# Kernel optimization log

Measured on AMD Instinct MI355X. Metric: run time of the kernel, lower is better.

The kernel has to match this reference:

```python
import jax, jax.numpy as jnp
import numpy as np

N_HEAD = 16
WINDOW = 16  # fixed_window_size


def setup_inputs() -> dict:
    key = jax.random.key(0)
    k1, k2, k3 = jax.random.split(key, 3)
    B, T, C = 2, 2048, 1024
    x = jax.random.normal(k1, (B, T, C), dtype=jnp.float32)
    # torch Linear(C, 3C, bias=False): y = x @ W.T with W [3C, C].
    # We store the pre-transposed [C, 3C] matrix so y = x @ w_qkv.
    w_qkv = jax.random.normal(k2, (C, 3 * C), dtype=jnp.float32) * (1.0 / np.sqrt(C))
    w_proj = jax.random.normal(k3, (C, C), dtype=jnp.float32) * (1.0 / np.sqrt(C))
    return {"x": x, "w_qkv": w_qkv, "w_proj": w_proj}


def reference(x, w_qkv, w_proj):
    B, T, C = x.shape
    H, D = N_HEAD, C // N_HEAD
    qkv = x @ w_qkv  # [B, T, 3C]
    q, k, v = jnp.split(qkv, 3, axis=-1)
    # [B, T, C] -> [B, H, T, D]
    q, k, v = (t.reshape(B, T, H, D).transpose(0, 2, 1, 3) for t in (q, k, v))
    att = jnp.einsum("bhtd,bhsd->bhts", q, k) * (1.0 / np.sqrt(D))  # [B,H,T,T]
    # Mask exactly as the torch module builds it: tril ones, then zero where
    # col - row >= fixed_window_size (note: col-row, per the source).
    row = jnp.arange(T)[:, None]
    col = jnp.arange(T)[None, :]
    mask = (col <= row) & ~(col - row >= WINDOW)  # [T, T] bool
    att = jnp.where(mask[None, None, :, :], att, -jnp.inf)
    att = jax.nn.softmax(att, axis=-1)
    y = jnp.einsum("bhts,bhsd->bhtd", att, v)  # [B,H,T,D]
    y = y.transpose(0, 2, 1, 3).reshape(B, T, C)
    return y @ w_proj
```

## Files before the change

### kernel.cpp

```cpp
#include <hip/hip_runtime.h>
#include <stdint.h>

#define LOG2E 1.4426950408889634f
#define QSCALE 0.18033688011112042f

typedef __attribute__((ext_vector_type(8))) short bf16x8;
typedef __attribute__((ext_vector_type(4))) float f32x4;
typedef __attribute__((ext_vector_type(8))) unsigned short u16x8;

#define B_ 2
#define T_ 2048
#define C_ 1024
#define H_ 16
#define D_ 64
#define BT_ 4096
#define N3_ 3072

#if __has_builtin(__builtin_amdgcn_exp2f)
#define EXP2(x) __builtin_amdgcn_exp2f(x)
#else
#define EXP2(x) exp2f(x)
#endif

__device__ __forceinline__ unsigned short f2bf(float f) {
  union { float f; unsigned u; } x; x.f = f;
  return (unsigned short)((x.u + 0x7fffu + ((x.u >> 16) & 1u)) >> 16);
}
__device__ __forceinline__ float bf2f(unsigned short u) {
  union { unsigned u; float f; } x; x.u = ((unsigned)u) << 16;
  return x.f;
}
__device__ __forceinline__ unsigned f2u(float f) {
  union { float f; unsigned u; } x; x.f = f; return x.u;
}
__device__ __forceinline__ unsigned pack_bf2(float a, float b) {
  return __builtin_amdgcn_perm(f2u(b) + 0x8000u, f2u(a) + 0x8000u, 0x07060302u);
}

__device__ __forceinline__ void gld16(const unsigned short* g, unsigned short* l) {
  __builtin_amdgcn_global_load_lds(
      (const __attribute__((address_space(1))) unsigned int*)g,
      (__attribute__((address_space(3))) unsigned int*)l, 16, 0, 0);
}

__device__ __forceinline__ void tr32(const float* __restrict__ in,
                                     unsigned short* __restrict__ out,
                                     int K, int N, int b, int nbx, int tid) {
  __shared__ unsigned short tile[32][33];
  const int bx = b % nbx, by = b / nbx;
  const int n0 = bx * 32, k0 = by * 32;
  const int tx = tid & 31, ty = (tid >> 5) * 4;
#pragma unroll
  for (int r = 0; r < 4; r++)
    tile[ty + r][tx] = f2bf(in[(size_t)(k0 + ty + r) * N + n0 + tx]);
  __syncthreads();
#pragma unroll
  for (int r = 0; r < 4; r++)
    out[(size_t)(n0 + ty + r) * K + k0 + tx] = tile[tx][ty + r];
}

__global__ __launch_bounds__(256) void prep_kernel(
    const float* __restrict__ x, unsigned short* __restrict__ xb,
    const float* __restrict__ wq, unsigned short* __restrict__ wqT,
    const float* __restrict__ wp, unsigned short* __restrict__ wpT) {
  const int bid = blockIdx.x, tid = threadIdx.x;
  if (bid < 4096) {
    int i = (bid * 256 + tid) * 4;
    float4 v = *(const float4*)(x + i);
    ushort4 o;
    o.x = f2bf(v.x); o.y = f2bf(v.y); o.z = f2bf(v.z); o.w = f2bf(v.w);
    *(ushort4*)(xb + i) = o;
  } else if (bid < 4096 + 3072) {
    tr32(wq, wqT, 1024, 3072, bid - 4096, 96, tid);
  } else {
    tr32(wp, wpT, 1024, 1024, bid - 7168, 32, tid);
  }
}

__device__ __forceinline__ void stage128(const unsigned short* __restrict__ G,
                                         unsigned short* L, int k, int tid) {
#pragma unroll
  for (int j = 0; j < 2; j++) {
    const int s = tid + 512 * j;
    const int row = s >> 3, ch = s & 7;
    gld16(G + (size_t)row * 1024 + k + ((ch ^ (row & 7)) * 8), L + s * 8);
  }
}

__global__ __launch_bounds__(512, 2) void gemm1_kernel(
    const unsigned short* __restrict__ A, const unsigned short* __restrict__ Bt,
    unsigned short* __restrict__ qo, unsigned short* __restrict__ ko,
    unsigned short* __restrict__ vo) {
  __shared__ unsigned short As[2][256 * 64];
  __shared__ unsigned short Bs[2][256 * 64];
  const int tid = threadIdx.x;
  const int wid = tid >> 6, lane = tid & 63;
  const int quad = lane >> 4, l16 = lane & 15;
  const int wm = (wid >> 2) * 128, wn = (wid & 3) * 64;

  const int id = blockIdx.x;
  const int swz = (id & 7) * 24 + (id >> 3);
  const int mb = swz / 12, nb = swz % 12;
  const int m0 = mb * 256, n0 = nb * 256;

  f32x4 acc[8][4] = {};

  stage128(A + (size_t)m0 * 1024,         &As[0][0],    0, tid);
  stage128(A + (size_t)(m0 + 128) * 1024, &As[0][8192], 0, tid);
  stage128(Bt + (size_t)n0 * 1024,        &Bs[0][0],    0, tid);
  stage128(Bt + (size_t)(n0 + 128) * 1024,&Bs[0][8192], 0, tid);

  for (int kt = 0; kt < 16; kt++) {
    const int cur = kt & 1;
    const int knext = (kt + 1) * 64;
#pragma unroll
    for (int p = 0; p < 4; p++) {
      if (kt < 15) {
        if (p == 0)
          stage128(A + (size_t)m0 * 1024, &As[cur ^ 1][0], knext, tid);
        else if (p == 1)
          stage128(A + (size_t)(m0 + 128) * 1024, &As[cur ^ 1][8192], knext, tid);
        else if (p == 2)
          stage128(Bt + (size_t)n0 * 1024, &Bs[cur ^ 1][0], knext, tid);
        else
          stage128(Bt + (size_t)(n0 + 128) * 1024, &Bs[cur ^ 1][8192], knext, tid);
      }
      if (p == 0) {
        if (kt < 15) asm volatile("s_waitcnt vmcnt(2)" ::: "memory");
        else         asm volatile("s_waitcnt vmcnt(0)" ::: "memory");
      }
      __builtin_amdgcn_s_barrier();
      __builtin_amdgcn_sched_barrier(0);

      const int mh = p >> 1, nh = p & 1;
      bf16x8 af[4][2], bfr[2][2];
#pragma unroll
      for (int mi = 0; mi < 4; mi++) {
        const int row = wm + (mh * 4 + mi) * 16 + l16;
        const int sw = row & 7;
#pragma unroll
        for (int ks = 0; ks < 2; ks++)
          af[mi][ks] = *(const bf16x8*)(&As[cur][0] + row * 64 + (((ks * 4 + quad) ^ sw) * 8));
      }
#pragma unroll
      for (int ni = 0; ni < 2; ni++) {
        const int row = wn + (nh * 2 + ni) * 16 + l16;
        const int sw = row & 7;
#pragma unroll
        for (int ks = 0; ks < 2; ks++)
          bfr[ni][ks] = *(const bf16x8*)(&Bs[cur][0] + row * 64 + (((ks * 4 + quad) ^ sw) * 8));
      }

      __builtin_amdgcn_s_setprio(1);
#pragma unroll
      for (int ks = 0; ks < 2; ks++)
#pragma unroll
        for (int mi = 0; mi < 4; mi++)
#pragma unroll
          for (int ni = 0; ni < 2; ni++)
            acc[mh * 4 + mi][nh * 2 + ni] = __builtin_amdgcn_mfma_f32_16x16x32_bf16(
                af[mi][ks], bfr[ni][ks], acc[mh * 4 + mi][nh * 2 + ni], 0, 0, 0);
      __builtin_amdgcn_s_setprio(0);
      __builtin_amdgcn_s_barrier();
    }
  }

  const int part = n0 >> 10;
  const int hh = ((n0 + wn) >> 6) & 15;
#pragma unroll
  for (int mi8 = 0; mi8 < 8; mi8++) {
#pragma unroll
    for (int r = 0; r < 4; r++) {
      const int m = m0 + wm + mi8 * 16 + quad * 4 + r;
      const int b = m >> 11, t = m & 2047;
#pragma unroll
      for (int ni = 0; ni < 4; ni++) {
        const int d = ni * 16 + l16;
        float val = acc[mi8][ni][r];
        if (part == 0) val *= QSCALE;
        const unsigned short bv = f2bf(val);
        if (part == 0)
          qo[((size_t)(b * H_ + hh) * T_ + t) * D_ + d] = bv;
        else if (part == 1)
          ko[((size_t)(b * H_ + hh) * T_ + t) * D_ + d] = bv;
        else
          vo[((size_t)(b * H_ + hh) * D_ + d) * T_ + t] = bv;
      }
    }
  }
}

__global__ __launch_bounds__(512) void gemm2_kernel(
    const unsigned short* __restrict__ A, const unsigned short* __restrict__ Bt,
    float* __restrict__ fo) {
  __shared__ unsigned short As[2][128 * 64];
  __shared__ unsigned short Bs[2][64 * 64];
  const int tid = threadIdx.x;
  const int wave = tid >> 6, lane = tid & 63;
  const int quad = lane >> 4, l16 = lane & 15;
  const int grp = wave >> 2, w4 = wave & 3;
  const int wm = (w4 >> 1) * 64, wn = (w4 & 1) * 32;
  const int m0 = blockIdx.y * 128, n0 = blockIdx.x * 64;
  const int gtid = tid & 255;

  f32x4 acc[4][2] = {};
  const int kbase = grp * 512;
  unsigned short* Asg = &As[grp][0];
  unsigned short* Bsg = &Bs[grp][0];

  for (int kk = 0; kk < 512; kk += 64) {
    const int k = kbase + kk;
    __syncthreads();
#pragma unroll
    for (int i = 0; i < 4; i++) {
      const int s = gtid + 256 * i;
      const int row = s >> 3, ch = s & 7;
      gld16(A + (size_t)(m0 + row) * 1024 + k + ((ch ^ (row & 7)) * 8), Asg + s * 8);
    }
#pragma unroll
    for (int i = 0; i < 2; i++) {
      const int s = gtid + 256 * i;
      const int row = s >> 3, ch = s & 7;
      gld16(Bt + (size_t)(n0 + row) * 1024 + k + ((ch ^ (row & 7)) * 8), Bsg + s * 8);
    }
    __syncthreads();
#pragma unroll
    for (int sub = 0; sub < 2; sub++) {
      bf16x8 af[4], bfr[2];
#pragma unroll
      for (int mi = 0; mi < 4; mi++) {
        const int row = wm + mi * 16 + l16;
        af[mi] = *(const bf16x8*)(Asg + row * 64 + (((sub * 4 + quad) ^ (row & 7)) * 8));
      }
#pragma unroll
      for (int ni = 0; ni < 2; ni++) {
        const int row = wn + ni * 16 + l16;
        bfr[ni] = *(const bf16x8*)(Bsg + row * 64 + (((sub * 4 + quad) ^ (row & 7)) * 8));
      }
#pragma unroll
      for (int mi = 0; mi < 4; mi++)
#pragma unroll
        for (int ni = 0; ni < 2; ni++)
          acc[mi][ni] = __builtin_amdgcn_mfma_f32_16x16x32_bf16(af[mi], bfr[ni], acc[mi][ni], 0, 0, 0);
    }
  }

  __syncthreads();
  float* comb = (float*)&As[0][0];
  if (grp == 1) {
#pragma unroll
    for (int mi = 0; mi < 4; mi++)
#pragma unroll
      for (int ni = 0; ni < 2; ni++)
        *(f32x4*)(comb + ((w4 * 8 + mi * 2 + ni) * 256 + lane * 4)) = acc[mi][ni];
  }
  __syncthreads();
  if (grp == 0) {
#pragma unroll
    for (int mi = 0; mi < 4; mi++) {
#pragma unroll
      for (int ni = 0; ni < 2; ni++) {
        f32x4 oth = *(const f32x4*)(comb + ((w4 * 8 + mi * 2 + ni) * 256 + lane * 4));
        f32x4 v = acc[mi][ni] + oth;
#pragma unroll
        for (int r = 0; r < 4; r++) {
          const int m = m0 + wm + mi * 16 + quad * 4 + r;
          fo[(size_t)m * 1024 + n0 + wn + ni * 16 + l16] = v[r];
        }
      }
    }
  }
}

__global__ __launch_bounds__(256) void attn_kernel(
    const unsigned short* __restrict__ qb, const unsigned short* __restrict__ kb,
    const unsigned short* __restrict__ vb, unsigned short* __restrict__ yb,
    unsigned short* __restrict__ po, float* __restrict__ pl) {
  const int tid = threadIdx.x;
  const int wave = tid >> 6, lane = tid & 63;
  const int quad = lane >> 4, l16 = lane & 15;

  const int bid = blockIdx.x;
  const int bh = bid & 31;
  const int u = 62 - (bid >> 5);
  int qs, c, nch;
  if (u < 11) { qs = u; c = 0; nch = 1; }
  else if (u < 33) { int v = u - 11; qs = 11 + (v >> 1); c = v & 1; nch = 2; }
  else { int v = u - 33; qs = 22 + v / 3; c = v % 3; nch = 3; }
  const int nt = qs + 1;
  const int j0 = c * nt / nch, j1 = (c + 1) * nt / nch;
  const int b = bh >> 4, h = bh & 15;

  __shared__ unsigned short Ks[64 * 64];
  __shared__ unsigned short Vt[64 * 64];
  __shared__ unsigned short Ps[4 * 16 * 68];
  unsigned short* Pw = Ps + wave * 16 * 68;

  const unsigned short* Qg = qb + (size_t)bh * T_ * D_;
  const unsigned short* Kg = kb + (size_t)bh * T_ * D_;
  const unsigned short* Vg = vb + (size_t)bh * D_ * T_;

  const unsigned short* qp = Qg + (size_t)(qs * 64 + wave * 16 + l16) * D_ + quad * 8;
  bf16x8 qf0 = *(const bf16x8*)qp, qf1 = *(const bf16x8*)(qp + 32);

  f32x4 o[4] = {};
  float lacc = 0.f;
  const int qglob = qs * 64 + wave * 16 + l16;
  const int sloc_base = quad * 4;

  const int trow = tid >> 3, tch = tid & 7;

  for (int jt = j0; jt < j1; jt++) {
    const int s0 = jt * 64;
    __syncthreads();
    {
      const int r0 = trow, r1 = trow + 32;
      gld16(Kg + (size_t)(s0 + r0) * D_ + ((tch ^ (r0 & 7)) * 8), Ks + r0 * 64 + tch * 8);
      gld16(Kg + (size_t)(s0 + r1) * D_ + ((tch ^ (r1 & 7)) * 8), Ks + r1 * 64 + tch * 8);
      gld16(Vg + (size_t)r0 * T_ + s0 + ((tch ^ (r0 & 7)) * 8), Vt + r0 * 64 + tch * 8);
      gld16(Vg + (size_t)r1 * T_ + s0 + ((tch ^ (r1 & 7)) * 8), Vt + r1 * 64 + tch * 8);
    }
    __syncthreads();

    f32x4 s[4];
#pragma unroll
    for (int mi = 0; mi < 4; mi++) {
      const int row = mi * 16 + l16, sw = row & 7;
      bf16x8 kf0 = *(const bf16x8*)(Ks + row * 64 + ((quad ^ sw) * 8));
      bf16x8 kf1 = *(const bf16x8*)(Ks + row * 64 + (((quad + 4) ^ sw) * 8));
      f32x4 z = {0.f, 0.f, 0.f, 0.f};
      z = __builtin_amdgcn_mfma_f32_16x16x32_bf16(kf0, qf0, z, 0, 0, 0);
      s[mi] = __builtin_amdgcn_mfma_f32_16x16x32_bf16(kf1, qf1, z, 0, 0, 0);
    }

    if (jt == qs) {
#pragma unroll
      for (int mi = 0; mi < 4; mi++)
#pragma unroll
        for (int r = 0; r < 4; r++) {
          float p = EXP2(s[mi][r]);
          p = (s0 + mi * 16 + sloc_base + r > qglob) ? 0.f : p;
          s[mi][r] = p;
          lacc += p;
        }
    } else {
#pragma unroll
      for (int mi = 0; mi < 4; mi++)
#pragma unroll
        for (int r = 0; r < 4; r++) {
          float p = EXP2(s[mi][r]);
          s[mi][r] = p;
          lacc += p;
        }
    }

#pragma unroll
    for (int mi = 0; mi < 4; mi++) {
      unsigned d0 = pack_bf2(s[mi][0], s[mi][1]);
      unsigned d1 = pack_bf2(s[mi][2], s[mi][3]);
      *(uint2*)(Pw + l16 * 68 + mi * 16 + quad * 4) = make_uint2(d0, d1);
    }

#pragma unroll
    for (int kk = 0; kk < 2; kk++) {
      bf16x8 pf = *(const bf16x8*)(Pw + l16 * 68 + kk * 32 + quad * 8);
#pragma unroll
      for (int ni = 0; ni < 4; ni++) {
        const int row = ni * 16 + l16, sw = row & 7;
        bf16x8 vf = *(const bf16x8*)(Vt + row * 64 + (((kk * 4 + quad) ^ sw) * 8));
        o[ni] = __builtin_amdgcn_mfma_f32_16x16x32_bf16(pf, vf, o[ni], 0, 0, 0);
      }
    }
  }

  lacc += __shfl_xor(lacc, 16, 64);
  lacc += __shfl_xor(lacc, 32, 64);
  float lr[4];
#pragma unroll
  for (int r = 0; r < 4; r++) lr[r] = __shfl(lacc, quad * 4 + r, 16);

  if (nch == 1) {
#pragma unroll
    for (int r = 0; r < 4; r++) {
      float inv = 1.0f / lr[r];
      int tq = qs * 64 + wave * 16 + quad * 4 + r;
#pragma unroll
      for (int ni = 0; ni < 4; ni++)
        yb[((size_t)(b * T_ + tq)) * 1024 + h * 64 + ni * 16 + l16] = f2bf(o[ni][r] * inv);
    }
  } else {
    const int slot = 52 * bh + ((qs <= 21) ? ((qs - 11) * 2 + c) : (22 + (qs - 22) * 3 + c));
    unsigned short* pob = po + (size_t)slot * 4096;
#pragma unroll
    for (int r = 0; r < 4; r++) {
      const int row64 = wave * 16 + quad * 4 + r;
#pragma unroll
      for (int ni = 0; ni < 4; ni++)
        pob[row64 * 64 + ni * 16 + l16] = f2bf(o[ni][r]);
      if (l16 == 0) pl[slot * 64 + row64] = lr[r];
    }
  }
}

__global__ __launch_bounds__(256) void reduce_kernel(
    const unsigned short* __restrict__ po, const float* __restrict__ pl,
    unsigned short* __restrict__ yb) {
  int idx = blockIdx.x * 256 + threadIdx.x;
  int bh = idx / 21504;
  int rem = idx - bh * 21504;
  int rr = rem >> 4, cg = rem & 15;
  int qs = 11 + (rr >> 6), row64 = rr & 63;
  int base, nch;
  if (qs <= 21) { base = (qs - 11) * 2; nch = 2; }
  else { base = 22 + (qs - 22) * 3; nch = 3; }
  int b = bh >> 4, h = bh & 15;
  float a0 = 0.f, a1 = 0.f, a2 = 0.f, a3 = 0.f, l = 0.f;
  for (int cc = 0; cc < nch; cc++) {
    int slot = 52 * bh + base + cc;
    const unsigned short* p = po + (size_t)slot * 4096 + row64 * 64 + cg * 4;
    ushort4 uv = *(const ushort4*)p;
    a0 += bf2f(uv.x); a1 += bf2f(uv.y); a2 += bf2f(uv.z); a3 += bf2f(uv.w);
    l += pl[slot * 64 + row64];
  }
  float inv = 1.0f / l;
  int tq = qs * 64 + row64;
  ushort4 w;
  w.x = f2bf(a0 * inv); w.y = f2bf(a1 * inv); w.z = f2bf(a2 * inv); w.w = f2bf(a3 * inv);
  *(ushort4*)(yb + ((size_t)(b * T_ + tq)) * 1024 + h * 64 + cg * 4) = w;
}

extern "C" void kernel_launch(void* const* d_in, const int* in_sizes, int n_in,
                              void* d_out, int out_size, void* d_ws, size_t ws_size,
                              hipStream_t stream) {
  const float* x = (const float*)d_in[0];
  const float* w_qkv = (const float*)d_in[1];
  const float* w_proj = (const float*)d_in[2];
  float* out = (float*)d_out;

  unsigned short* xb = (unsigned short*)d_ws;
  unsigned short* wprojT = xb + (size_t)BT_ * C_;
  unsigned short* qb = wprojT + (size_t)C_ * C_;
  unsigned short* kb = qb + (size_t)B_ * H_ * T_ * D_;
  unsigned short* vb = kb + (size_t)B_ * H_ * T_ * D_;
  unsigned short* wqkvT = vb + (size_t)B_ * H_ * T_ * D_;
  unsigned short* po = wqkvT;
  float* pl = (float*)(po + (size_t)1664 * 4096);
  unsigned short* yb = xb;

  prep_kernel<<<dim3(8192), 256, 0, stream>>>(x, xb, w_qkv, wqkvT, w_proj, wprojT);

  gemm1_kernel<<<dim3(192), 512, 0, stream>>>(xb, wqkvT, qb, kb, vb);
  attn_kernel<<<dim3(32 * 63), 256, 0, stream>>>(qb, kb, vb, yb, po, pl);
  reduce_kernel<<<dim3(2688), 256, 0, stream>>>(po, pl, yb);
  gemm2_kernel<<<dim3(C_ / 64, BT_ / 128), 512, 0, stream>>>(yb, wprojT, out);
}
```

Measured before the change: 215.7 us.

## Restructure QKV GEMM K-loop: issue full next-tile prefetch once, reuse fragments across quadrants

The QKV projection GEMM main loop now issues all global-to-LDS loads for the next K tile at the start of each iteration, followed by one wait and barrier pair. Previously the loads were spread over four sub-phases, each with its own barriers. The four MFMA quadrants are now visited in a snake order (00,01,11,10) so that A or B fragments loaded from LDS are reused between adjacent quadrants. This cuts the number of LDS reads and barriers per K step. In exchange, the loads are issued in one burst rather than interleaved with compute, and fragments stay live in registers longer.

```diff
diff --git a/kernel.cpp b/kernel.cpp
--- a/kernel.cpp
+++ b/kernel.cpp
@@ -87,6 +87,54 @@
   }
 }
 
+__device__ __forceinline__ void stage_tile(const unsigned short* __restrict__ A,
+                                           const unsigned short* __restrict__ Bt,
+                                           int m0, int n0, int k,
+                                           unsigned short* as, unsigned short* bs, int tid) {
+  stage128(A + (size_t)m0 * 1024,          as,        k, tid);
+  stage128(A + (size_t)(m0 + 128) * 1024,  as + 8192, k, tid);
+  stage128(Bt + (size_t)n0 * 1024,         bs,        k, tid);
+  stage128(Bt + (size_t)(n0 + 128) * 1024, bs + 8192, k, tid);
+}
+
+template <int H>
+__device__ __forceinline__ void load_a4(bf16x8 f[4][2], const unsigned short* base,
+                                        int w0, int l16, int quad) {
+#pragma unroll
+  for (int i = 0; i < 4; i++) {
+    const int row = w0 + (H * 4 + i) * 16 + l16;
+    const int sw = row & 7;
+#pragma unroll
+    for (int ks = 0; ks < 2; ks++)
+      f[i][ks] = *(const bf16x8*)(base + row * 64 + (((ks * 4 + quad) ^ sw) * 8));
+  }
+}
+template <int H>
+__device__ __forceinline__ void load_b2(bf16x8 f[2][2], const unsigned short* base,
+                                        int w0, int l16, int quad) {
+#pragma unroll
+  for (int i = 0; i < 2; i++) {
+    const int row = w0 + (H * 2 + i) * 16 + l16;
+    const int sw = row & 7;
+#pragma unroll
+    for (int ks = 0; ks < 2; ks++)
+      f[i][ks] = *(const bf16x8*)(base + row * 64 + (((ks * 4 + quad) ^ sw) * 8));
+  }
+}
+template <int MH, int NH>
+__device__ __forceinline__ void mfma_quad(f32x4 acc[8][4], bf16x8 af[4][2], bf16x8 bfr[2][2]) {
+  __builtin_amdgcn_s_setprio(1);
+#pragma unroll
+  for (int ks = 0; ks < 2; ks++)
+#pragma unroll
+    for (int mi = 0; mi < 4; mi++)
+#pragma unroll
+      for (int ni = 0; ni < 2; ni++)
+        acc[MH * 4 + mi][NH * 2 + ni] = __builtin_amdgcn_mfma_f32_16x16x32_bf16(
+            af[mi][ks], bfr[ni][ks], acc[MH * 4 + mi][NH * 2 + ni], 0, 0, 0);
+  __builtin_amdgcn_s_setprio(0);
+}
+
 __global__ __launch_bounds__(512, 2) void gemm1_kernel(
     const unsigned short* __restrict__ A, const unsigned short* __restrict__ Bt,
     unsigned short* __restrict__ qo, unsigned short* __restrict__ ko,
@@ -105,64 +153,33 @@
 
   f32x4 acc[8][4] = {};
 
-  stage128(A + (size_t)m0 * 1024,         &As[0][0],    0, tid);
-  stage128(A + (size_t)(m0 + 128) * 1024, &As[0][8192], 0, tid);
-  stage128(Bt + (size_t)n0 * 1024,        &Bs[0][0],    0, tid);
-  stage128(Bt + (size_t)(n0 + 128) * 1024,&Bs[0][8192], 0, tid);
+  stage_tile(A, Bt, m0, n0, 0, &As[0][0], &Bs[0][0], tid);
 
   for (int kt = 0; kt < 16; kt++) {
     const int cur = kt & 1;
-    const int knext = (kt + 1) * 64;
-#pragma unroll
-    for (int p = 0; p < 4; p++) {
-      if (kt < 15) {
-        if (p == 0)
-          stage128(A + (size_t)m0 * 1024, &As[cur ^ 1][0], knext, tid);
-        else if (p == 1)
-          stage128(A + (size_t)(m0 + 128) * 1024, &As[cur ^ 1][8192], knext, tid);
-        else if (p == 2)
-          stage128(Bt + (size_t)n0 * 1024, &Bs[cur ^ 1][0], knext, tid);
-        else
-          stage128(Bt + (size_t)(n0 + 128) * 1024, &Bs[cur ^ 1][8192], knext, tid);
-      }
-      if (p == 0) {
-        if (kt < 15) asm volatile("s_waitcnt vmcnt(2)" ::: "memory");
-        else         asm volatile("s_waitcnt vmcnt(0)" ::: "memory");
-      }
-      __builtin_amdgcn_s_barrier();
-      __builtin_amdgcn_sched_barrier(0);
-
-      const int mh = p >> 1, nh = p & 1;
-      bf16x8 af[4][2], bfr[2][2];
-#pragma unroll
-      for (int mi = 0; mi < 4; mi++) {
-        const int row = wm + (mh * 4 + mi) * 16 + l16;
-        const int sw = row & 7;
-#pragma unroll
-        for (int ks = 0; ks < 2; ks++)
-          af[mi][ks] = *(const bf16x8*)(&As[cur][0] + row * 64 + (((ks * 4 + quad) ^ sw) * 8));
-      }
-#pragma unroll
-      for (int ni = 0; ni < 2; ni++) {
-        const int row = wn + (nh * 2 + ni) * 16 + l16;
-        const int sw = row & 7;
-#pragma unroll
-        for (int ks = 0; ks < 2; ks++)
-          bfr[ni][ks] = *(const bf16x8*)(&Bs[cur][0] + row * 64 + (((ks * 4 + quad) ^ sw) * 8));
-      }
-
-      __builtin_amdgcn_s_setprio(1);
-#pragma unroll
-      for (int ks = 0; ks < 2; ks++)
-#pragma unroll
-        for (int mi = 0; mi < 4; mi++)
-#pragma unroll
-          for (int ni = 0; ni < 2; ni++)
-            acc[mh * 4 + mi][nh * 2 + ni] = __builtin_amdgcn_mfma_f32_16x16x32_bf16(
-                af[mi][ks], bfr[ni][ks], acc[mh * 4 + mi][nh * 2 + ni], 0, 0, 0);
-      __builtin_amdgcn_s_setprio(0);
-      __builtin_amdgcn_s_barrier();
-    }
+    const unsigned short* as = &As[cur][0];
+    const unsigned short* bs = &Bs[cur][0];
+
+    __builtin_amdgcn_s_barrier();
+    if (kt < 15) {
+      stage_tile(A, Bt, m0, n0, (kt + 1) * 64, &As[cur ^ 1][0], &Bs[cur ^ 1][0], tid);
+      asm volatile("s_waitcnt vmcnt(8)" ::: "memory");
+    } else {
+      asm volatile("s_waitcnt vmcnt(0)" ::: "memory");
+    }
+    __builtin_amdgcn_s_barrier();
+    __builtin_amdgcn_sched_barrier(0);
+
+    bf16x8 af[4][2], bfr[2][2];
+    load_a4<0>(af, as, wm, l16, quad);
+    load_b2<0>(bfr, bs, wn, l16, quad);
+    mfma_quad<0, 0>(acc, af, bfr);
+    load_b2<1>(bfr, bs, wn, l16, quad);
+    mfma_quad<0, 1>(acc, af, bfr);
+    load_a4<1>(af, as, wm, l16, quad);
+    mfma_quad<1, 1>(acc, af, bfr);
+    load_b2<0>(bfr, bs, wn, l16, quad);
+    mfma_quad<1, 0>(acc, af, bfr);
   }
 
   const int part = n0 >> 10;
```

After: 205.9 us. 1.05x faster.
